# Performance work log

Measured on AMD Instinct MI355X. Metric: run time of the kernel, lower is better.

The kernel has to match this reference:

```python
import jax, jax.numpy as jnp
import numpy as np

N = 50000      # n_nodes
S = 16         # neighbors per node
D_IN = 256     # raw feature dim
PREP = 128     # prep_len
H = 2          # n_head
OUT = 64       # per-head spec output_dim (concat_node doubles it)
MP = 2         # n_mp (metapaths)
IN2 = 2 * OUT * H  # layer-2 input dim = 256


def setup_inputs() -> dict:
    key = jax.random.key(0)
    ks = jax.random.split(key, 7)
    feats = jax.random.normal(ks[0], (N, D_IN), jnp.float32)
    prep_W = jax.random.normal(ks[1], (D_IN, PREP), jnp.float32) * 0.05
    Wx1 = jax.random.normal(ks[2], (MP, H, PREP, OUT), jnp.float32) * 0.05
    Wn1 = jax.random.normal(ks[3], (MP, H, PREP, OUT), jnp.float32) * 0.05
    Wx2 = jax.random.normal(ks[4], (MP, H, IN2, OUT), jnp.float32) * 0.05
    Wn2 = jax.random.normal(ks[5], (MP, H, IN2, OUT), jnp.float32) * 0.05
    node_neigh = jax.random.randint(ks[6], (MP, N, S), 0, N, dtype=jnp.int32)
    return {"feats": feats, "prep_W": prep_W, "Wx1": Wx1, "Wn1": Wn1,
            "Wx2": Wx2, "Wn2": Wn2, "node_neigh": node_neigh}


def _agg_layer(x, neigh, Wx, Wn):
    # x: [N, d]; neigh: [N, S]; Wx, Wn: [H, d, OUT]
    # neighbor gather + mean (the chunk_edge = all_feats[node_neigh] path)
    agg = jnp.mean(x[neigh], axis=1)                  # [N, d]
    xh = jnp.einsum('nd,hdo->nho', x, Wx)             # [N, H, OUT]
    nh = jnp.einsum('nd,hdo->nho', agg, Wn)           # [N, H, OUT]
    h = jax.nn.relu(jnp.concatenate([xh, nh], -1))    # per-head concat_node
    return h.reshape(x.shape[0], -1)                  # heads concatenated


def reference(feats, prep_W, Wx1, Wn1, Wx2, Wn2, node_neigh):
    # feats[all_ids].detach() in the original -> stop_gradient
    feats = jax.lax.stop_gradient(feats)
    outs = []
    for mp in range(MP):
        h0 = feats @ prep_W                           # prep (dummy == layer-1 prep here)
        neigh = node_neigh[mp]
        h1 = _agg_layer(h0, neigh, Wx1[mp], Wn1[mp])  # [N, 256]
        h2 = _agg_layer(h1, neigh, Wx2[mp], Wn2[mp])  # [N, 256]
        outs.append(jnp.concatenate([h1, h2], axis=-1))  # skip-buffer concat
    return jnp.stack(outs, axis=0)                    # [MP, N, 512]
```

## Files before the change

### kernel.cpp

```cpp
#include <hip/hip_runtime.h>

#define NN 50000
#define SNEI 16
#define GB 782

typedef unsigned short ushort_t;
typedef unsigned int uint_t;
typedef unsigned long long u64;
typedef __attribute__((ext_vector_type(8))) short bhalf8;
typedef __attribute__((ext_vector_type(4))) float facc4;
typedef __attribute__((ext_vector_type(4))) float f32x4;
typedef __attribute__((ext_vector_type(4))) int i32x4;
typedef __attribute__((ext_vector_type(4))) uint_t u32x4;

__device__ __forceinline__ float b2f(uint_t u) {
    union { uint_t u; float f; } x; x.u = u << 16; return x.f;
}
__device__ __forceinline__ ushort_t f2b(float f) {
    union { float f; uint_t u; } x; x.f = f;
    return (ushort_t)((x.u + 0x7FFFu + ((x.u >> 16) & 1u)) >> 16);
}
__device__ __forceinline__ u64 pack4(float a, float b, float c, float d) {
    return (u64)f2b(a) | ((u64)f2b(b) << 16) | ((u64)f2b(c) << 32) | ((u64)f2b(d) << 48);
}

typedef const __attribute__((address_space(1))) void cglb_t;
typedef __attribute__((address_space(3))) void lds3_t;
__device__ __forceinline__ void gload16(const void* g, void* l) {
    __builtin_amdgcn_global_load_lds((cglb_t*)g, (lds3_t*)l, 16, 0, 0);
}

__global__ void permSetup(const float* __restrict__ prepW,
                          const float* __restrict__ Wx1, const float* __restrict__ Wn1,
                          const float* __restrict__ Wx2, const float* __restrict__ Wn2,
                          ushort_t* __restrict__ dst)
{
    int e = blockIdx.x * 256 + threadIdx.x;
    int q8 = e >> 3, j = e & 7;
    int layer = q8 >> 14;
    int qq = q8 & 16383;
    int mp = qq >> 13, isN = (qq >> 12) & 1, q = qq & 4095;
    int lane = q & 63, nf = (q >> 6) & 7, ks = q >> 9;
    int c = nf * 16 + (lane & 15);
    int k = ks * 32 + ((lane >> 4) << 3) + j;
    float v;
    if (layer == 0) {
        const float* W1 = (isN ? Wn1 : Wx1) + mp * 16384 + (c >> 6) * 8192 + (c & 63);
        const float* pw = prepW + (size_t)k * 128;
        float s0 = 0.f, s1 = 0.f;
#pragma unroll 4
        for (int p = 0; p < 128; p += 2) {
            s0 += pw[p]     * W1[(size_t)p * 64];
            s1 += pw[p + 1] * W1[(size_t)(p + 1) * 64];
        }
        v = s0 + s1;
    } else {
        const float* W2 = (isN ? Wn2 : Wx2) + mp * 32768 + (c >> 6) * 16384 + (size_t)k * 64 + (c & 63);
        v = *W2;
    }
    dst[(size_t)q8 * 8 + j] = f2b(v);
}

template<bool NTX>
__global__ __launch_bounds__(256, 4)
void proj_gemm(const float* __restrict__ X, int xPitch, size_t xMpStr,
               const ushort_t* __restrict__ W, size_t wMpStr,
               float* __restrict__ out, size_t oMpStr, int obase,
               ushort_t* __restrict__ P, size_t PMpStr)
{
    __shared__ bhalf8 lds[2560];
    u64* l64 = (u64*)lds;
    const int tid = threadIdx.x;
    const int lane = tid & 63;
    const int wid = tid >> 6;
    const int wave_m = wid >> 1, wave_n = wid & 1;
    const int m0 = blockIdx.x * 64;
    const int mp = blockIdx.y;

    const float* Xp = X + (size_t)mp * xMpStr;
    const ushort_t* wx = W + (size_t)mp * wMpStr;
    const ushort_t* wn = wx + 4096 * 8;
    float* outp = out + (size_t)mp * oMpStr;
    ushort_t* Pp = P + (size_t)mp * PMpStr;

    facc4 acc[2][8];
    const facc4 z = {0.f, 0.f, 0.f, 0.f};
#pragma unroll
    for (int i = 0; i < 2; ++i)
#pragma unroll
        for (int j = 0; j < 8; ++j) acc[i][j] = z;

    for (int kt = 0; kt < 4; ++kt) {
#pragma unroll
        for (int it = 0; it < 2; ++it) {
            int s = tid + it * 256;
            int fp = s >> 6, ls = s & 63;
            int mf = fp & 3, ksl = fp >> 2;
            int row = m0 + mf * 16 + (ls & 15); if (row > NN - 1) row = NN - 1;
            const f32x4* gp = (const f32x4*)(Xp + (size_t)row * xPitch + kt * 64 + ksl * 32 + ((ls >> 4) << 3));
            f32x4 f0, f1;
            if constexpr (NTX) { f0 = __builtin_nontemporal_load(gp); f1 = __builtin_nontemporal_load(gp + 1); }
            else               { f0 = gp[0]; f1 = gp[1]; }
            l64[s * 2]     = pack4(f0[0], f0[1], f0[2], f0[3]);
            l64[s * 2 + 1] = pack4(f1[0], f1[1], f1[2], f1[3]);
        }
#pragma unroll
        for (int it = 0; it < 4; ++it) {
            int cb = (it * 4 + wid) * 64;
            gload16(wx + ((size_t)kt * 1024 + cb + lane) * 8,
                    (char*)lds + (512 + cb + lane) * 16);
            gload16(wn + ((size_t)kt * 1024 + cb + lane) * 8,
                    (char*)lds + (1536 + cb + lane) * 16);
        }
        __syncthreads();
        const int wB = wave_n ? 1536 : 512;
#pragma unroll
        for (int ksl = 0; ksl < 2; ++ksl) {
            bhalf8 a0 = lds[(ksl * 4 + wave_m * 2 + 0) * 64 + lane];
            bhalf8 a1 = lds[(ksl * 4 + wave_m * 2 + 1) * 64 + lane];
#pragma unroll
            for (int nf = 0; nf < 8; ++nf) {
                bhalf8 b = lds[wB + (ksl * 8 + nf) * 64 + lane];
                acc[0][nf] = __builtin_amdgcn_mfma_f32_16x16x32_bf16(a0, b, acc[0][nf], 0, 0, 0);
                acc[1][nf] = __builtin_amdgcn_mfma_f32_16x16x32_bf16(a1, b, acc[1][nf], 0, 0, 0);
            }
        }
        __syncthreads();
    }
    const int cl = lane & 15, rg = lane >> 4;
    float* xl = (float*)lds;
    if (wave_n == 0) {
#pragma unroll
        for (int mf2 = 0; mf2 < 2; ++mf2) {
            int rowl = (wave_m * 2 + mf2) * 16 + rg * 4;
#pragma unroll
            for (int nf = 0; nf < 8; ++nf) {
                int cpr = nf * 16 + cl;
                facc4 v = acc[mf2][nf];
#pragma unroll
                for (int rr = 0; rr < 4; ++rr)
                    xl[(rowl + rr) * 132 + cpr] = fmaxf(v[rr], 0.0f);
            }
        }
    } else {
#pragma unroll
        for (int mf2 = 0; mf2 < 2; ++mf2) {
            int rowb = m0 + (wave_m * 2 + mf2) * 16 + rg * 4;
#pragma unroll
            for (int nf = 0; nf < 8; ++nf) {
                int cpr = nf * 16 + cl;
                facc4 v = acc[mf2][nf];
#pragma unroll
                for (int rr = 0; rr < 4; ++rr) {
                    int row = rowb + rr;
                    if (row < NN)
                        Pp[(size_t)(cpr >> 5) * (NN * 32) + (size_t)row * 32 + (cpr & 31)] = f2b(v[rr]);
                }
            }
        }
    }
    __syncthreads();
    {
#pragma unroll
        for (int j = 0; j < 4; ++j) {
            int rowl = wid * 16 + j * 4 + rg / 1;
            int rowl2 = wid * 16 + j * 4 + (lane >> 4);
            int row = m0 + rowl2;
            (void)rowl;
#pragma unroll
            for (int c = 0; c < 2; ++c) {
                int base = rowl2 * 132 + c * 64 + cl * 4;
                f32x4 v = *(f32x4*)&xl[base];
                if (row < NN)
                    __builtin_nontemporal_store(v,
                        (f32x4*)&outp[(size_t)row * 512 + obase + c * 128 + cl * 4]);
            }
        }
    }
}

__global__ __launch_bounds__(256)
void gatherS(const ushort_t* __restrict__ P, size_t PMpStr,
             const int* __restrict__ nb, size_t nMpStr,
             float* __restrict__ out, size_t oMpStr,
             int obase, int shift)
{
    const int b = blockIdx.x;
    const int pair = b & ((1 << shift) - 1);
    const int slice = pair & 3, mp = pair >> 2;
    const int nodeBase = (b >> shift) * 64;

    const ushort_t* Pp = P + (size_t)mp * PMpStr + (size_t)slice * (NN * 32);
    const int* nbp = nb + (size_t)mp * nMpStr;
    float* outp = out + (size_t)mp * oMpStr;

    __shared__ int nls[1024];
    __shared__ float og[64 * 36];
    {
        int i4 = nodeBase * 4 + threadIdx.x;
        int mx = NN * 4 - 1;
        if (i4 > mx) i4 = mx;
        i32x4 v = __builtin_nontemporal_load((const i32x4*)nbp + i4);
        ((i32x4*)nls)[threadIdx.x] = v;
    }
    __syncthreads();

    const int nl = threadIdx.x >> 2, q = threadIdx.x & 3;
    const int* nr = nls + nl * SNEI;
    float a0=0.f,a1=0.f,a2=0.f,a3=0.f,a4=0.f,a5=0.f,a6=0.f,a7=0.f;
#pragma unroll
    for (int s = 0; s < SNEI; ++s) {
        u32x4 v = *(const u32x4*)(Pp + (size_t)nr[s] * 32 + q * 8);
        a0 += b2f(v.x & 0xFFFFu); a1 += b2f(v.x >> 16);
        a2 += b2f(v.y & 0xFFFFu); a3 += b2f(v.y >> 16);
        a4 += b2f(v.z & 0xFFFFu); a5 += b2f(v.z >> 16);
        a6 += b2f(v.w & 0xFFFFu); a7 += b2f(v.w >> 16);
    }
    const float M = 0.0625f;
    f32x4 r0 = { fmaxf(a0*M, 0.f), fmaxf(a1*M, 0.f), fmaxf(a2*M, 0.f), fmaxf(a3*M, 0.f) };
    f32x4 r1 = { fmaxf(a4*M, 0.f), fmaxf(a5*M, 0.f), fmaxf(a6*M, 0.f), fmaxf(a7*M, 0.f) };
    *(f32x4*)&og[nl * 36 + q * 8]     = r0;
    *(f32x4*)&og[nl * 36 + q * 8 + 4] = r1;
    __syncthreads();

    const int coff0 = (slice >> 1) * 128 + 64 + (slice & 1) * 32;
#pragma unroll
    for (int it = 0; it < 2; ++it) {
        int rl = it * 32 + (threadIdx.x >> 3), sub = threadIdx.x & 7;
        int node = nodeBase + rl;
        f32x4 v = *(f32x4*)&og[rl * 36 + sub * 4];
        if (node < NN)
            __builtin_nontemporal_store(v,
                (f32x4*)(outp + (size_t)node * 512 + obase + coff0 + sub * 4));
    }
}

extern "C" void kernel_launch(void* const* d_in, const int* in_sizes, int n_in,
                              void* d_out, int out_size, void* d_ws, size_t ws_size,
                              hipStream_t stream)
{
    const float* feats  = (const float*)d_in[0];
    const float* prepWp = (const float*)d_in[1];
    const float* Wx1    = (const float*)d_in[2];
    const float* Wn1    = (const float*)d_in[3];
    const float* Wx2    = (const float*)d_in[4];
    const float* Wn2    = (const float*)d_in[5];
    const int*   neigh  = (const int*)d_in[6];
    float* out = (float*)d_out;
    ushort_t* ws = (ushort_t*)d_ws;

    const size_t permElems = 262144;
    const size_t needBatched = (permElems + 2 * (size_t)NN * 128) * 2;
    const bool batched = ws_size >= needBatched;
    const int nmp = batched ? 2 : 1;

    ushort_t* perm = ws;
    ushort_t* P    = ws + permElems;

    permSetup<<<1024, 256, 0, stream>>>(prepWp, Wx1, Wn1, Wx2, Wn2, perm);

    const size_t PStr = batched ? (size_t)NN * 128 : 0;
    const size_t oStr = batched ? (size_t)NN * 512 : 0;
    const size_t nStr = batched ? (size_t)NN * SNEI : 0;
    const size_t wStr = batched ? (size_t)8192 * 8 : 0;
    const int shift = batched ? 3 : 2;
    const int passes = batched ? 1 : 2;

    for (int p = 0; p < passes; ++p) {
        const ushort_t* w1 = perm + (size_t)p * 8192 * 8;
        const ushort_t* w2 = perm + (size_t)(16384 + p * 8192) * 8;
        float* outp = out + (size_t)p * NN * 512;
        const int* nbp = neigh + (size_t)p * NN * SNEI;
        dim3 gp(GB, nmp);
        const int gg = GB << shift;

        proj_gemm<false><<<gp, 256, 0, stream>>>(feats, 256, 0,
                                                 w1, wStr, outp, oStr, 0, P, PStr);
        gatherS<<<gg, 256, 0, stream>>>(P, PStr, nbp, nStr, outp, oStr, 0, shift);

        proj_gemm<true><<<gp, 256, 0, stream>>>(outp, 512, oStr,
                                                w2, wStr, outp, oStr, 256, P, PStr);
        gatherS<<<gg, 256, 0, stream>>>(P, PStr, nbp, nStr, outp, oStr, 256, shift);
    }
}
```

Before: 181.5 us.

## Share feats load across metapaths and stage h1 as bf16 for layer-2 GEMM

Layer-1 projection now runs as one 512-thread kernel that loads each feats tile once and computes all four metapath/role weight products, instead of reading feats once per metapath. Layer-1 outputs, from both the GEMM and the gather, are also written as a bf16 copy into workspace. The layer-2 GEMM reads that bf16 copy with direct 16-byte loads rather than reloading and converting fp32 from the output buffer. This adds extra bf16 writes and needs more workspace, and the small-workspace fallback path is removed.

New measurement: 173.7 us. 1.05x faster.

```diff
diff --git a/kernel.cpp b/kernel.cpp
--- a/kernel.cpp
+++ b/kernel.cpp
@@ -61,15 +61,121 @@
     dst[(size_t)q8 * 8 + j] = f2b(v);
 }
 
-template<bool NTX>
+__global__ __launch_bounds__(512, 4)
+void proj1_gemm(const float* __restrict__ X,
+                const ushort_t* __restrict__ W, size_t wMpStr,
+                float* __restrict__ out, size_t oMpStr,
+                ushort_t* __restrict__ h1, size_t hMpStr,
+                ushort_t* __restrict__ P, size_t PMpStr)
+{
+    __shared__ bhalf8 lds[4608];
+    u64* l64 = (u64*)lds;
+    const int tid = threadIdx.x;
+    const int lane = tid & 63;
+    const int wid = tid >> 6;
+    const int wave_m = wid >> 2;
+    const int role = wid & 3;
+    const int mp = role >> 1, isN = role & 1;
+    const int m0 = blockIdx.x * 64;
+
+    facc4 acc[2][8];
+    const facc4 z = {0.f, 0.f, 0.f, 0.f};
+#pragma unroll
+    for (int i = 0; i < 2; ++i)
+#pragma unroll
+        for (int j = 0; j < 8; ++j) acc[i][j] = z;
+
+    for (int kt = 0; kt < 4; ++kt) {
+        {
+            int s = tid;
+            int fp = s >> 6, ls = s & 63;
+            int mf = fp & 3, ksl = fp >> 2;
+            int row = m0 + mf * 16 + (ls & 15); if (row > NN - 1) row = NN - 1;
+            const f32x4* gp = (const f32x4*)(X + (size_t)row * 256 + kt * 64 + ksl * 32 + ((ls >> 4) << 3));
+            f32x4 f0 = gp[0], f1 = gp[1];
+            l64[s * 2]     = pack4(f0[0], f0[1], f0[2], f0[3]);
+            l64[s * 2 + 1] = pack4(f1[0], f1[1], f1[2], f1[3]);
+        }
+#pragma unroll
+        for (int it = 0; it < 8; ++it) {
+            int c4 = it * 512 + tid;
+            int m = c4 >> 10, c = c4 & 1023;
+            const ushort_t* src = W + (size_t)(m >> 1) * wMpStr + (m & 1) * 32768
+                                + ((size_t)kt * 1024 + c) * 8;
+            gload16(src, (char*)lds + (512 + m * 1024 + c) * 16);
+        }
+        __syncthreads();
+        const int wB = 512 + role * 1024;
+#pragma unroll
+        for (int ksl = 0; ksl < 2; ++ksl) {
+            bhalf8 a0 = lds[(ksl * 4 + wave_m * 2 + 0) * 64 + lane];
+            bhalf8 a1 = lds[(ksl * 4 + wave_m * 2 + 1) * 64 + lane];
+#pragma unroll
+            for (int nf = 0; nf < 8; ++nf) {
+                bhalf8 b = lds[wB + (ksl * 8 + nf) * 64 + lane];
+                acc[0][nf] = __builtin_amdgcn_mfma_f32_16x16x32_bf16(a0, b, acc[0][nf], 0, 0, 0);
+                acc[1][nf] = __builtin_amdgcn_mfma_f32_16x16x32_bf16(a1, b, acc[1][nf], 0, 0, 0);
+            }
+        }
+        __syncthreads();
+    }
+    const int cl = lane & 15, rg = lane >> 4;
+    if (isN == 0) {
+        float* xl = (float*)lds + mp * (64 * 132);
+#pragma unroll
+        for (int mf2 = 0; mf2 < 2; ++mf2) {
+            int rowl = (wave_m * 2 + mf2) * 16 + rg * 4;
+#pragma unroll
+            for (int nf = 0; nf < 8; ++nf) {
+                int cpr = nf * 16 + cl;
+                facc4 v = acc[mf2][nf];
+#pragma unroll
+                for (int rr = 0; rr < 4; ++rr)
+                    xl[(rowl + rr) * 132 + cpr] = fmaxf(v[rr], 0.0f);
+            }
+        }
+    } else {
+        ushort_t* Pp = P + (size_t)mp * PMpStr;
+#pragma unroll
+        for (int mf2 = 0; mf2 < 2; ++mf2) {
+            int rowb = m0 + (wave_m * 2 + mf2) * 16 + rg * 4;
+#pragma unroll
+            for (int nf = 0; nf < 8; ++nf) {
+                int cpr = nf * 16 + cl;
+                facc4 v = acc[mf2][nf];
+#pragma unroll
+                for (int rr = 0; rr < 4; ++rr) {
+                    int row = rowb + rr;
+                    if (row < NN)
+                        Pp[(size_t)(cpr >> 5) * (NN * 32) + (size_t)row * 32 + (cpr & 31)] = f2b(v[rr]);
+                }
+            }
+        }
+    }
+    __syncthreads();
+#pragma unroll
+    for (int it = 0; it < 8; ++it) {
+        int u = it * 512 + tid;
+        int seg = u >> 4, l16 = u & 15;
+        int mp2 = seg >> 7, rowl = (seg >> 1) & 63, ch = seg & 1;
+        int row = m0 + rowl;
+        f32x4 v = *(f32x4*)((float*)lds + mp2 * (64 * 132) + rowl * 132 + ch * 64 + l16 * 4);
+        if (row < NN) {
+            __builtin_nontemporal_store(v,
+                (f32x4*)(out + (size_t)mp2 * oMpStr + (size_t)row * 512 + ch * 128 + l16 * 4));
+            *(u64*)(h1 + (size_t)mp2 * hMpStr + (size_t)row * 256 + ch * 128 + l16 * 4)
+                = pack4(v[0], v[1], v[2], v[3]);
+        }
+    }
+}
+
 __global__ __launch_bounds__(256, 4)
-void proj_gemm(const float* __restrict__ X, int xPitch, size_t xMpStr,
-               const ushort_t* __restrict__ W, size_t wMpStr,
-               float* __restrict__ out, size_t oMpStr, int obase,
-               ushort_t* __restrict__ P, size_t PMpStr)
+void proj2_gemm(const ushort_t* __restrict__ X, size_t xMpStr,
+                const ushort_t* __restrict__ W, size_t wMpStr,
+                float* __restrict__ out, size_t oMpStr,
+                ushort_t* __restrict__ P, size_t PMpStr)
 {
     __shared__ bhalf8 lds[2560];
-    u64* l64 = (u64*)lds;
     const int tid = threadIdx.x;
     const int lane = tid & 63;
     const int wid = tid >> 6;
@@ -77,7 +183,7 @@
     const int m0 = blockIdx.x * 64;
     const int mp = blockIdx.y;
 
-    const float* Xp = X + (size_t)mp * xMpStr;
+    const ushort_t* Xp = X + (size_t)mp * xMpStr;
     const ushort_t* wx = W + (size_t)mp * wMpStr;
     const ushort_t* wn = wx + 4096 * 8;
     float* outp = out + (size_t)mp * oMpStr;
@@ -93,16 +199,11 @@
     for (int kt = 0; kt < 4; ++kt) {
 #pragma unroll
         for (int it = 0; it < 2; ++it) {
-            int s = tid + it * 256;
-            int fp = s >> 6, ls = s & 63;
-            int mf = fp & 3, ksl = fp >> 2;
-            int row = m0 + mf * 16 + (ls & 15); if (row > NN - 1) row = NN - 1;
-            const f32x4* gp = (const f32x4*)(Xp + (size_t)row * xPitch + kt * 64 + ksl * 32 + ((ls >> 4) << 3));
-            f32x4 f0, f1;
-            if constexpr (NTX) { f0 = __builtin_nontemporal_load(gp); f1 = __builtin_nontemporal_load(gp + 1); }
-            else               { f0 = gp[0]; f1 = gp[1]; }
-            l64[s * 2]     = pack4(f0[0], f0[1], f0[2], f0[3]);
-            l64[s * 2 + 1] = pack4(f1[0], f1[1], f1[2], f1[3]);
+            int u = wid + it * 4;
+            int mf = u & 3, ksl = u >> 2;
+            int row = m0 + mf * 16 + (lane & 15); if (row > NN - 1) row = NN - 1;
+            const ushort_t* src = Xp + (size_t)row * 256 + kt * 64 + ksl * 32 + ((lane >> 4) << 3);
+            gload16(src, (char*)lds + (u * 64 + lane) * 16);
         }
 #pragma unroll
         for (int it = 0; it < 4; ++it) {
@@ -160,35 +261,31 @@
         }
     }
     __syncthreads();
-    {
-#pragma unroll
-        for (int j = 0; j < 4; ++j) {
-            int rowl = wid * 16 + j * 4 + rg / 1;
-            int rowl2 = wid * 16 + j * 4 + (lane >> 4);
-            int row = m0 + rowl2;
-            (void)rowl;
-#pragma unroll
-            for (int c = 0; c < 2; ++c) {
-                int base = rowl2 * 132 + c * 64 + cl * 4;
-                f32x4 v = *(f32x4*)&xl[base];
-                if (row < NN)
-                    __builtin_nontemporal_store(v,
-                        (f32x4*)&outp[(size_t)row * 512 + obase + c * 128 + cl * 4]);
-            }
-        }
-    }
-}
-
+#pragma unroll
+    for (int j = 0; j < 4; ++j) {
+        int rowl2 = wid * 16 + j * 4 + (lane >> 4);
+        int row = m0 + rowl2;
+#pragma unroll
+        for (int c = 0; c < 2; ++c) {
+            f32x4 v = *(f32x4*)&xl[rowl2 * 132 + c * 64 + cl * 4];
+            if (row < NN)
+                __builtin_nontemporal_store(v,
+                    (f32x4*)&outp[(size_t)row * 512 + 256 + c * 128 + cl * 4]);
+        }
+    }
+}
+
+template<bool WRH1>
 __global__ __launch_bounds__(256)
 void gatherS(const ushort_t* __restrict__ P, size_t PMpStr,
              const int* __restrict__ nb, size_t nMpStr,
-             float* __restrict__ out, size_t oMpStr,
-             int obase, int shift)
+             float* __restrict__ out, size_t oMpStr, int obase,
+             ushort_t* __restrict__ h1, size_t hMpStr)
 {
     const int b = blockIdx.x;
-    const int pair = b & ((1 << shift) - 1);
+    const int pair = b & 7;
     const int slice = pair & 3, mp = pair >> 2;
-    const int nodeBase = (b >> shift) * 64;
+    const int nodeBase = (b >> 3) * 64;
 
     const ushort_t* Pp = P + (size_t)mp * PMpStr + (size_t)slice * (NN * 32);
     const int* nbp = nb + (size_t)mp * nMpStr;
@@ -206,6 +303,7 @@
     __syncthreads();
 
     const int nl = threadIdx.x >> 2, q = threadIdx.x & 3;
+    const int node = nodeBase + nl;
     const int* nr = nls + nl * SNEI;
     float a0=0.f,a1=0.f,a2=0.f,a3=0.f,a4=0.f,a5=0.f,a6=0.f,a7=0.f;
 #pragma unroll
@@ -219,6 +317,14 @@
     const float M = 0.0625f;
     f32x4 r0 = { fmaxf(a0*M, 0.f), fmaxf(a1*M, 0.f), fmaxf(a2*M, 0.f), fmaxf(a3*M, 0.f) };
     f32x4 r1 = { fmaxf(a4*M, 0.f), fmaxf(a5*M, 0.f), fmaxf(a6*M, 0.f), fmaxf(a7*M, 0.f) };
+    const int cco = (slice >> 1) * 128 + 64 + (slice & 1) * 32 + q * 8;
+    if constexpr (WRH1) {
+        if (node < NN) {
+            ushort_t* hp = h1 + (size_t)mp * hMpStr + (size_t)node * 256 + cco;
+            *(u64*)hp       = pack4(r0[0], r0[1], r0[2], r0[3]);
+            *(u64*)(hp + 4) = pack4(r1[0], r1[1], r1[2], r1[3]);
+        }
+    }
     *(f32x4*)&og[nl * 36 + q * 8]     = r0;
     *(f32x4*)&og[nl * 36 + q * 8 + 4] = r1;
     __syncthreads();
@@ -227,11 +333,11 @@
 #pragma unroll
     for (int it = 0; it < 2; ++it) {
         int rl = it * 32 + (threadIdx.x >> 3), sub = threadIdx.x & 7;
-        int node = nodeBase + rl;
+        int nd = nodeBase + rl;
         f32x4 v = *(f32x4*)&og[rl * 36 + sub * 4];
-        if (node < NN)
+        if (nd < NN)
             __builtin_nontemporal_store(v,
-                (f32x4*)(outp + (size_t)node * 512 + obase + coff0 + sub * 4));
+                (f32x4*)(outp + (size_t)nd * 512 + obase + coff0 + sub * 4));
     }
 }
 
@@ -250,36 +356,25 @@
     ushort_t* ws = (ushort_t*)d_ws;
 
     const size_t permElems = 262144;
-    const size_t needBatched = (permElems + 2 * (size_t)NN * 128) * 2;
-    const bool batched = ws_size >= needBatched;
-    const int nmp = batched ? 2 : 1;
-
     ushort_t* perm = ws;
     ushort_t* P    = ws + permElems;
+    ushort_t* h1   = P + 2 * (size_t)NN * 128;
+
+    const size_t PStr = (size_t)NN * 128;
+    const size_t hStr = (size_t)NN * 256;
+    const size_t oStr = (size_t)NN * 512;
+    const size_t nStr = (size_t)NN * SNEI;
+    const size_t wStr = (size_t)8192 * 8;
 
     permSetup<<<1024, 256, 0, stream>>>(prepWp, Wx1, Wn1, Wx2, Wn2, perm);
 
-    const size_t PStr = batched ? (size_t)NN * 128 : 0;
-    const size_t oStr = batched ? (size_t)NN * 512 : 0;
-    const size_t nStr = batched ? (size_t)NN * SNEI : 0;
-    const size_t wStr = batched ? (size_t)8192 * 8 : 0;
-    const int shift = batched ? 3 : 2;
-    const int passes = batched ? 1 : 2;
-
-    for (int p = 0; p < passes; ++p) {
-        const ushort_t* w1 = perm + (size_t)p * 8192 * 8;
-        const ushort_t* w2 = perm + (size_t)(16384 + p * 8192) * 8;
-        float* outp = out + (size_t)p * NN * 512;
-        const int* nbp = neigh + (size_t)p * NN * SNEI;
-        dim3 gp(GB, nmp);
-        const int gg = GB << shift;
-
-        proj_gemm<false><<<gp, 256, 0, stream>>>(feats, 256, 0,
-                                                 w1, wStr, outp, oStr, 0, P, PStr);
-        gatherS<<<gg, 256, 0, stream>>>(P, PStr, nbp, nStr, outp, oStr, 0, shift);
-
-        proj_gemm<true><<<gp, 256, 0, stream>>>(outp, 512, oStr,
-                                                w2, wStr, outp, oStr, 256, P, PStr);
-        gatherS<<<gg, 256, 0, stream>>>(P, PStr, nbp, nStr, outp, oStr, 256, shift);
-    }
-}
+    proj1_gemm<<<GB, 512, 0, stream>>>(feats, perm, wStr,
+                                       out, oStr, h1, hStr, P, PStr);
+    gatherS<true><<<GB * 8, 256, 0, stream>>>(P, PStr, neigh, nStr,
+                                              out, oStr, 0, h1, hStr);
+    proj2_gemm<<<dim3(GB, 2), 256, 0, stream>>>(h1, hStr,
+                                                perm + (size_t)16384 * 8, wStr,
+                                                out, oStr, P, PStr);
+    gatherS<false><<<GB * 8, 256, 0, stream>>>(P, PStr, neigh, nStr,
+                                               out, oStr, 256, nullptr, 0);
+}
```
